# Kernel tuning notes

Hardware: AMD Instinct MI355X
Metric: run time of the kernel (lower is better)

## Reference

```python
import jax, jax.numpy as jnp
import numpy as np

B, R, N, F = 8, 8, 1024, 256


def setup_inputs() -> dict:
    key = jax.random.key(0)
    k1, k2 = jax.random.split(key)
    inputs = jax.random.normal(k1, (B, R, N, F), dtype=jnp.float32)
    Bs = jax.random.normal(k2, (R, F, F), dtype=jnp.float32) * 0.05
    return {"inputs": inputs, "Bs": Bs}


def reference(inputs, Bs):
    # E_r @ B_r : [B,R,N,F] x [R,F,F] -> [B,R,N,F]
    e = jnp.einsum("brnf,rfg->brng", inputs, Bs)
    # (E_r B_r) @ E_r^T : [B,R,N,F] x [B,R,M,F] -> [B,R,N,M]
    scores = jnp.einsum("brng,brmg->brnm", e, inputs)
    return jax.nn.sigmoid(scores)
```

## Files before the change

### kernel.cpp

```cpp
#include <hip/hip_runtime.h>


typedef float    f32x4 __attribute__((ext_vector_type(4)));
typedef _Float16 f16x8 __attribute__((ext_vector_type(8)));
typedef _Float16 f16x4 __attribute__((ext_vector_type(4)));

#define WS_E_OFF   0
#define WS_BST_OFF 16777216

__global__ __launch_bounds__(256) void bl_convert(
    const float* __restrict__ E, const float* __restrict__ Bs,
    _Float16* __restrict__ wsE, _Float16* __restrict__ wsBsT) {
  int bid = blockIdx.x, tid = threadIdx.x;
  if (bid < 8192) {
    int cid = (bid << 8) + tid;
    int br  = cid >> 15;
    int rem = cid & 32767;
    int fc  = rem >> 10;
    int n   = rem & 1023;
    const float* src = E + ((size_t)br << 18) + n * 256 + (fc << 3);
    f32x4 v0 = *(const f32x4*)src;
    f32x4 v1 = *(const f32x4*)(src + 4);
    f16x8 h;
    h[0] = (_Float16)v0[0]; h[1] = (_Float16)v0[1];
    h[2] = (_Float16)v0[2]; h[3] = (_Float16)v0[3];
    h[4] = (_Float16)v1[0]; h[5] = (_Float16)v1[1];
    h[6] = (_Float16)v1[2]; h[7] = (_Float16)v1[3];
    *(f16x8*)(wsE + ((size_t)br << 18) + (fc << 13) + (n << 3)) = h;
  } else {
    int cid = ((bid - 8192) << 8) + tid;
    int r   = cid >> 13;
    int rem = cid & 8191;
    int fc  = rem >> 8;
    int g   = rem & 255;
    const float* src = Bs + (r << 16) + (fc << 3) * 256 + g;
    f16x8 h;
#pragma unroll
    for (int j = 0; j < 8; ++j) h[j] = (_Float16)src[j * 256];
    *(f16x8*)(wsBsT + (r << 16) + (fc << 11) + (g << 3)) = h;
  }
}

__global__ __launch_bounds__(512, 2) void bl_fused(
    const _Float16* __restrict__ wsE, const _Float16* __restrict__ wsBsT,
    float* __restrict__ out) {
  __shared__ _Float16 se[32768];
  __shared__ _Float16 stg[24576];
  int b0  = blockIdx.x;
  int bid = ((b0 & 7) << 6) + (b0 >> 3);
  int br  = bid >> 3;
  int nb  = bid & 7;
  int n0  = nb << 7;
  int r   = br & 7;
  int tid = threadIdx.x;
  int lane = tid & 63, wave = tid >> 6;
  int quad = lane >> 4, l16 = lane & 15;

  const _Float16* eG  = wsE + ((size_t)br << 18);
  const _Float16* bsG = wsBsT + (r << 16);

  {
    int wg  = wave >> 1;
    int wnn = wave & 1;
    f32x4 acc[4][4] = {};
    for (int kk = 0; kk < 4; ++kk) {
      f16x8 va[2], vb[4];
#pragma unroll
      for (int i = 0; i < 2; ++i) {
        int c = (i << 9) + tid;
        int kcl = c >> 7, nl = c & 127;
        va[i] = *(const f16x8*)(eG + (((kk << 3) + kcl) << 13) + ((n0 + nl) << 3));
      }
#pragma unroll
      for (int i = 0; i < 4; ++i) {
        int c = (i << 9) + tid;
        int kcl = c >> 8, gl = c & 255;
        vb[i] = *(const f16x8*)(bsG + (((kk << 3) + kcl) << 11) + (gl << 3));
      }
      __syncthreads();
#pragma unroll
      for (int i = 0; i < 2; ++i) {
        int c = (i << 9) + tid;
        *(f16x8*)&stg[c << 3] = va[i];
      }
#pragma unroll
      for (int i = 0; i < 4; ++i) {
        int c = (i << 9) + tid;
        *(f16x8*)&stg[8192 + (c << 3)] = vb[i];
      }
      __syncthreads();
#pragma unroll
      for (int ks = 0; ks < 2; ++ks) {
        int kc = (ks << 2) + quad;
        f16x8 af[4], bf[4];
#pragma unroll
        for (int rt = 0; rt < 4; ++rt)
          af[rt] = *(const f16x8*)&stg[((kc << 7) + (wnn << 6) + (rt << 4) + l16) << 3];
#pragma unroll
        for (int ct = 0; ct < 4; ++ct)
          bf[ct] = *(const f16x8*)&stg[8192 + (((kc << 8) + (wg << 6) + (ct << 4) + l16) << 3)];
#pragma unroll
        for (int rt = 0; rt < 4; ++rt)
#pragma unroll
          for (int ct = 0; ct < 4; ++ct)
            acc[rt][ct] = __builtin_amdgcn_mfma_f32_16x16x32_f16(bf[ct], af[rt], acc[rt][ct], 0, 0, 0);
      }
    }
#pragma unroll
    for (int rt = 0; rt < 4; ++rt) {
      int n = (wnn << 6) + (rt << 4) + l16;
#pragma unroll
      for (int ct = 0; ct < 4; ++ct) {
        int g  = (wg << 6) + (ct << 4) + (quad << 2);
        int gc = g >> 3, gj = g & 7;
        f16x4 h;
#pragma unroll
        for (int i = 0; i < 4; ++i) h[i] = (_Float16)acc[rt][ct][i];
        *(f16x4*)&se[(gc << 10) + (n << 3) + gj] = h;
      }
    }
  }

  int mw0 = (wave >> 1) << 7;
  int nn  = (wave & 1) << 6;

  f32x4 acc2[8][4] = {};
  f16x8 bf[2][8];

#pragma unroll
  for (int mf = 0; mf < 8; ++mf)
    bf[0][mf] = *(const f16x8*)(eG + (quad << 13) + ((mw0 + (mf << 4) + l16) << 3));

  __syncthreads();

  float* oB = out + ((size_t)br << 20);
#pragma unroll
  for (int g = 0; g < 16; ++g) {
    const int p  = g & 1;
    const int mt = g >> 3;
    if (g < 15) {
      const int g2   = g + 1;
      const int kcb2 = (((g2 >> 1) & 3) << 3) + ((g2 & 1) << 2);
      const int mb2  = ((g2 >> 3) << 9) + mw0;
#pragma unroll
      for (int mf = 0; mf < 8; ++mf)
        bf[p ^ 1][mf] = *(const f16x8*)(eG + ((kcb2 + quad) << 13) + ((mb2 + (mf << 4) + l16) << 3));
    }
    const int kcq = (((g >> 1) & 3) << 3) + ((g & 1) << 2) + quad;
    f16x8 af[4];
#pragma unroll
    for (int rt = 0; rt < 4; ++rt)
      af[rt] = *(const f16x8*)&se[((kcq << 7) + nn + (rt << 4) + l16) << 3];
#pragma unroll
    for (int mf = 0; mf < 8; ++mf)
#pragma unroll
      for (int rt = 0; rt < 4; ++rt)
        acc2[mf][rt] = __builtin_amdgcn_mfma_f32_16x16x32_f16(bf[p][mf], af[rt], acc2[mf][rt], 0, 0, 0);
    if (g == 7 || g == 15) {
      const int mb = (mt << 9) + mw0 + (quad << 2);
#pragma unroll
      for (int mf = 0; mf < 8; ++mf) {
#pragma unroll
        for (int rt = 0; rt < 4; ++rt) {
          int n = n0 + nn + (rt << 4) + l16;
          f32x4 v;
#pragma unroll
          for (int i = 0; i < 4; ++i)
            v[i] = __builtin_amdgcn_rcpf(1.0f + __expf(-acc2[mf][rt][i]));
          *(f32x4*)(oB + ((size_t)n << 10) + mb + (mf << 4)) = v;
          acc2[mf][rt] = (f32x4){0.f, 0.f, 0.f, 0.f};
        }
      }
    }
  }
}

extern "C" void kernel_launch(void* const* d_in, const int* in_sizes, int n_in,
                              void* d_out, int out_size, void* d_ws, size_t ws_size,
                              hipStream_t stream) {
  const float* E  = (const float*)d_in[0];
  const float* Bs = (const float*)d_in[1];
  _Float16* wsE   = (_Float16*)d_ws + WS_E_OFF;
  _Float16* wsBsT = (_Float16*)d_ws + WS_BST_OFF;
  float* out = (float*)d_out;

  bl_convert<<<8448, 256, 0, stream>>>(E, Bs, wsE, wsBsT);
  bl_fused<<<512, 512, 0, stream>>>(wsE, wsBsT, out);
}
```

Baseline: 393.4 us.

## Drop LDS staging, read operands from global, shrink tiles for higher occupancy

The first GEMM now loads E and Bs^T fragments directly from global memory into registers, so the shared staging buffer and its barriers are gone. The second GEMM switches from an 8x4 accumulator tile with double-buffered prefetch to four passes of 4x4 tiles. The launch bound rises from 2 to 4 blocks per CU. The aim is to cut LDS use and register pressure so more waves stay resident and hide latency. In exchange there are more redundant global/L2 reads, less reuse per load, and no explicit software prefetch.

```diff
diff --git a/kernel.cpp b/kernel.cpp
--- a/kernel.cpp
+++ b/kernel.cpp
@@ -41,11 +41,10 @@
   }
 }
 
-__global__ __launch_bounds__(512, 2) void bl_fused(
+__global__ __launch_bounds__(512, 4) void bl_fused(
     const _Float16* __restrict__ wsE, const _Float16* __restrict__ wsBsT,
     float* __restrict__ out) {
   __shared__ _Float16 se[32768];
-  __shared__ _Float16 stg[24576];
   int b0  = blockIdx.x;
   int bid = ((b0 & 7) << 6) + (b0 >> 3);
   int br  = bid >> 3;
@@ -55,56 +54,29 @@
   int tid = threadIdx.x;
   int lane = tid & 63, wave = tid >> 6;
   int quad = lane >> 4, l16 = lane & 15;
+  int wg  = wave >> 1;
+  int wnn = wave & 1;
 
   const _Float16* eG  = wsE + ((size_t)br << 18);
   const _Float16* bsG = wsBsT + (r << 16);
 
   {
-    int wg  = wave >> 1;
-    int wnn = wave & 1;
     f32x4 acc[4][4] = {};
-    for (int kk = 0; kk < 4; ++kk) {
-      f16x8 va[2], vb[4];
 #pragma unroll
-      for (int i = 0; i < 2; ++i) {
-        int c = (i << 9) + tid;
-        int kcl = c >> 7, nl = c & 127;
-        va[i] = *(const f16x8*)(eG + (((kk << 3) + kcl) << 13) + ((n0 + nl) << 3));
-      }
+    for (int kq = 0; kq < 8; ++kq) {
+      int kc = (kq << 2) + quad;
+      f16x8 af[4], bf[4];
 #pragma unroll
-      for (int i = 0; i < 4; ++i) {
-        int c = (i << 9) + tid;
-        int kcl = c >> 8, gl = c & 255;
-        vb[i] = *(const f16x8*)(bsG + (((kk << 3) + kcl) << 11) + (gl << 3));
-      }
-      __syncthreads();
+      for (int rt = 0; rt < 4; ++rt)
+        af[rt] = *(const f16x8*)(eG + (kc << 13) + ((n0 + (wnn << 6) + (rt << 4) + l16) << 3));
 #pragma unroll
-      for (int i = 0; i < 2; ++i) {
-        int c = (i << 9) + tid;
-        *(f16x8*)&stg[c << 3] = va[i];
-      }
+      for (int ct = 0; ct < 4; ++ct)
+        bf[ct] = *(const f16x8*)(bsG + (kc << 11) + (((wg << 6) + (ct << 4) + l16) << 3));
 #pragma unroll
-      for (int i = 0; i < 4; ++i) {
-        int c = (i << 9) + tid;
-        *(f16x8*)&stg[8192 + (c << 3)] = vb[i];
-      }
-      __syncthreads();
-#pragma unroll
-      for (int ks = 0; ks < 2; ++ks) {
-        int kc = (ks << 2) + quad;
-        f16x8 af[4], bf[4];
-#pragma unroll
-        for (int rt = 0; rt < 4; ++rt)
-          af[rt] = *(const f16x8*)&stg[((kc << 7) + (wnn << 6) + (rt << 4) + l16) << 3];
+      for (int rt = 0; rt < 4; ++rt)
 #pragma unroll
         for (int ct = 0; ct < 4; ++ct)
-          bf[ct] = *(const f16x8*)&stg[8192 + (((kc << 8) + (wg << 6) + (ct << 4) + l16) << 3)];
-#pragma unroll
-        for (int rt = 0; rt < 4; ++rt)
-#pragma unroll
-          for (int ct = 0; ct < 4; ++ct)
-            acc[rt][ct] = __builtin_amdgcn_mfma_f32_16x16x32_f16(bf[ct], af[rt], acc[rt][ct], 0, 0, 0);
-      }
+          acc[rt][ct] = __builtin_amdgcn_mfma_f32_16x16x32_f16(bf[ct], af[rt], acc[rt][ct], 0, 0, 0);
     }
 #pragma unroll
     for (int rt = 0; rt < 4; ++rt) {
@@ -121,55 +93,40 @@
     }
   }
 
-  int mw0 = (wave >> 1) << 7;
-  int nn  = (wave & 1) << 6;
-
-  f32x4 acc2[8][4] = {};
-  f16x8 bf[2][8];
-
-#pragma unroll
-  for (int mf = 0; mf < 8; ++mf)
-    bf[0][mf] = *(const f16x8*)(eG + (quad << 13) + ((mw0 + (mf << 4) + l16) << 3));
-
   __syncthreads();
 
   float* oB = out + ((size_t)br << 20);
 #pragma unroll
-  for (int g = 0; g < 16; ++g) {
-    const int p  = g & 1;
-    const int mt = g >> 3;
-    if (g < 15) {
-      const int g2   = g + 1;
-      const int kcb2 = (((g2 >> 1) & 3) << 3) + ((g2 & 1) << 2);
-      const int mb2  = ((g2 >> 3) << 9) + mw0;
+  for (int mp = 0; mp < 4; ++mp) {
+    int m0p = (mp << 8) + (wg << 6);
+    f32x4 acc[4][4] = {};
 #pragma unroll
-      for (int mf = 0; mf < 8; ++mf)
-        bf[p ^ 1][mf] = *(const f16x8*)(eG + ((kcb2 + quad) << 13) + ((mb2 + (mf << 4) + l16) << 3));
-    }
-    const int kcq = (((g >> 1) & 3) << 3) + ((g & 1) << 2) + quad;
-    f16x8 af[4];
+    for (int kq = 0; kq < 8; ++kq) {
+      int kc = (kq << 2) + quad;
+      f16x8 af[4], bf[4];
 #pragma unroll
-    for (int rt = 0; rt < 4; ++rt)
-      af[rt] = *(const f16x8*)&se[((kcq << 7) + nn + (rt << 4) + l16) << 3];
-#pragma unroll
-    for (int mf = 0; mf < 8; ++mf)
+      for (int ct = 0; ct < 4; ++ct)
+        bf[ct] = *(const f16x8*)(eG + (kc << 13) + ((m0p + (ct << 4) + l16) << 3));
 #pragma unroll
       for (int rt = 0; rt < 4; ++rt)
-        acc2[mf][rt] = __builtin_amdgcn_mfma_f32_16x16x32_f16(bf[p][mf], af[rt], acc2[mf][rt], 0, 0, 0);
-    if (g == 7 || g == 15) {
-      const int mb = (mt << 9) + mw0 + (quad << 2);
+        af[rt] = *(const f16x8*)&se[((kc << 7) + (wnn << 6) + (rt << 4) + l16) << 3];
 #pragma unroll
-      for (int mf = 0; mf < 8; ++mf) {
+      for (int ct = 0; ct < 4; ++ct)
 #pragma unroll
-        for (int rt = 0; rt < 4; ++rt) {
-          int n = n0 + nn + (rt << 4) + l16;
-          f32x4 v;
+        for (int rt = 0; rt < 4; ++rt)
+          acc[ct][rt] = __builtin_amdgcn_mfma_f32_16x16x32_f16(bf[ct], af[rt], acc[ct][rt], 0, 0, 0);
+    }
 #pragma unroll
-          for (int i = 0; i < 4; ++i)
-            v[i] = __builtin_amdgcn_rcpf(1.0f + __expf(-acc2[mf][rt][i]));
-          *(f32x4*)(oB + ((size_t)n << 10) + mb + (mf << 4)) = v;
-          acc2[mf][rt] = (f32x4){0.f, 0.f, 0.f, 0.f};
-        }
+    for (int ct = 0; ct < 4; ++ct) {
+#pragma unroll
+      for (int rt = 0; rt < 4; ++rt) {
+        int n = n0 + (wnn << 6) + (rt << 4) + l16;
+        int m = m0p + (ct << 4) + (quad << 2);
+        f32x4 v;
+#pragma unroll
+        for (int i = 0; i < 4; ++i)
+          v[i] = __builtin_amdgcn_rcpf(1.0f + __expf(-acc[ct][rt][i]));
+        *(f32x4*)(oB + ((size_t)n << 10) + m) = v;
       }
     }
   }
```

New measurement: 409.8 us. +4.2%, slower.
